# Performance work log

Measured on AMD Instinct MI355X. Metric: run time of the kernel, lower is better.

Reference implementation:

```python
import jax, jax.numpy as jnp
import numpy as np

TAU = 2.0      # LIF membrane time constant
ALPHA = 4.0    # sigmoid surrogate sharpness (spikingjelly default)
EPS = 1e-5     # BatchNorm eps
HEADS = 8


def lif(x, vth):
    """MultiStepLIFNode: scan over leading time dim T. Hard reset to 0, detach_reset.
    Forward spike = heaviside(h - vth); backward uses sigmoid surrogate via straight-through."""
    def step(v, xt):
        h = v + (xt - v) / TAU
        hv = h - vth
        sg = jax.nn.sigmoid(ALPHA * hv)
        hard = (hv >= 0).astype(h.dtype)
        spike = sg + jax.lax.stop_gradient(hard - sg)
        v_new = h * (1.0 - jax.lax.stop_gradient(spike))  # detach_reset=True, v_reset=0
        return v_new, spike
    _, spikes = jax.lax.scan(step, jnp.zeros_like(x[0]), x)
    return spikes


def bn(x, gamma, beta, mean, var):
    # x: (T,B,C,N), params: (C,) ; eval-mode BatchNorm1d over channel axis 2
    inv = (gamma * jax.lax.rsqrt(var + EPS))[None, None, :, None]
    return (x - mean[None, None, :, None]) * inv + beta[None, None, :, None]


def setup_inputs() -> dict:
    key = jax.random.key(0)
    T, B, C, H, W = 4, 16, 384, 32, 32
    ks = jax.random.split(key, 24)
    d = {"x": jax.random.normal(ks[0], (T, B, C, H, W), jnp.float32)}
    i = 1
    wscale = 1.0 / np.sqrt(C)
    for p in ("q", "k", "v", "p"):
        d[p + "_w"] = jax.random.normal(ks[i], (C, C), jnp.float32) * wscale; i += 1
        d[p + "_gamma"] = jax.random.uniform(ks[i], (C,), jnp.float32, 0.5, 1.5); i += 1
        d[p + "_beta"] = jax.random.normal(ks[i], (C,), jnp.float32) * 0.1; i += 1
        d[p + "_mean"] = jax.random.normal(ks[i], (C,), jnp.float32) * 0.1; i += 1
        d[p + "_var"] = jax.random.uniform(ks[i], (C,), jnp.float32, 0.5, 1.5); i += 1
    d["p_bias"] = jax.random.normal(ks[i], (C,), jnp.float32) * 0.1
    return d


def reference(x, q_w, q_gamma, q_beta, q_mean, q_var,
              k_w, k_gamma, k_beta, k_mean, k_var,
              v_w, v_gamma, v_beta, v_mean, v_var,
              p_w, p_bias, p_gamma, p_beta, p_mean, p_var):
    T, B, C, H, W = x.shape
    N = H * W
    Ch = C // HEADS
    # input spiking (named proj_lif in source, applied first)
    xs = lif(x, 1.0).reshape(T, B, C, N)

    def branch(w, g, b, m, v):
        y = jnp.einsum('tbcn,dc->tbdn', xs, w)  # 1x1 Conv1d == channel matmul
        return lif(bn(y, g, b, m, v), 1.0).reshape(T, B, HEADS, Ch, N)

    q = branch(q_w, q_gamma, q_beta, q_mean, q_var)
    k = branch(k_w, k_gamma, k_beta, k_mean, k_var)
    v = branch(v_w, v_gamma, v_beta, v_mean, v_var)

    attn = jnp.sum(k * v, axis=3, keepdims=True)  # (T,B,h,1,N)
    attn = lif(attn, 0.5)
    out = (q * attn).reshape(T, B, C, N)
    out = jnp.einsum('tbcn,dc->tbdn', out, p_w) + p_bias[None, None, :, None]
    out = bn(out, p_gamma, p_beta, p_mean, p_var)
    return out.reshape(T, B, C, H, W)
```

## Files before the change

kernel.cpp:

```cpp
#include <hip/hip_runtime.h>

typedef unsigned short u16;
typedef unsigned char u8;
typedef unsigned int u32;
typedef float f32x4 __attribute__((ext_vector_type(4)));
typedef __bf16 bf16x8 __attribute__((ext_vector_type(8)));

#define SPB 6291456

__device__ __forceinline__ void gll16(const void* g, void* l) {
  __builtin_amdgcn_global_load_lds((const __attribute__((address_space(1))) void*)g,
                                   (__attribute__((address_space(3))) void*)l, 16, 0, 0);
}

__device__ __forceinline__ uint4 expand8f(uint2 v, u32 t) {
  u32 a = (v.x >> t) & 0x01010101u;
  u32 b = (v.y >> t) & 0x01010101u;
  uint4 r;
  r.x = __builtin_amdgcn_perm(0u, a, 0x0C010C00u) * 0x3F80u;
  r.y = __builtin_amdgcn_perm(0u, a, 0x0C030C02u) * 0x3F80u;
  r.z = __builtin_amdgcn_perm(0u, b, 0x0C010C00u) * 0x3F80u;
  r.w = __builtin_amdgcn_perm(0u, b, 0x0C030C02u) * 0x3F80u;
  return r;
}

__global__ __launch_bounds__(256) void k_convert(
    const float* __restrict__ qw, const float* __restrict__ kw,
    const float* __restrict__ vw, const float* __restrict__ pw,
    const float* __restrict__ qg, const float* __restrict__ qbt,
    const float* __restrict__ qm, const float* __restrict__ qv,
    const float* __restrict__ kg, const float* __restrict__ kbt,
    const float* __restrict__ km, const float* __restrict__ kv,
    const float* __restrict__ vg, const float* __restrict__ vbt,
    const float* __restrict__ vm, const float* __restrict__ vv,
    const float* __restrict__ pg, const float* __restrict__ pbt,
    const float* __restrict__ pm, const float* __restrict__ pv,
    const float* __restrict__ pbias,
    u16* __restrict__ Wstk, u16* __restrict__ Pw,
    float4* __restrict__ BNP, float4* __restrict__ PP) {
  int tid = blockIdx.x * 256 + threadIdx.x;
  if (tid < 442368) {
    int r = tid / 384, c = tid - r * 384;
    const float* src = (r < 384) ? qw : (r < 768) ? kw : vw;
    int rr = (r >= 768) ? r - 768 : (r >= 384) ? r - 384 : r;
    unsigned int u = __float_as_uint(src[rr * 384 + c]);
    u = (u + 0x7FFFu + ((u >> 16) & 1u)) >> 16;
    Wstk[tid] = (u16)u;
  } else if (tid < 589824) {
    int i = tid - 442368;
    unsigned int u = __float_as_uint(pw[i]);
    u = (u + 0x7FFFu + ((u >> 16) & 1u)) >> 16;
    Pw[i] = (u16)u;
  } else if (tid < 590976) {
    int r = tid - 589824;
    int br = r / 384, ch = r - br * 384;
    const float* g  = (br == 0) ? qg  : (br == 1) ? kg  : vg;
    const float* bt = (br == 0) ? qbt : (br == 1) ? kbt : vbt;
    const float* m  = (br == 0) ? qm  : (br == 1) ? km  : vm;
    const float* va = (br == 0) ? qv  : (br == 1) ? kv  : vv;
    float inv = g[ch] / sqrtf(va[ch] + 1e-5f);
    BNP[r] = make_float4(inv, m[ch], bt[ch], 0.f);
  } else if (tid < 591360) {
    int ch = tid - 590976;
    float inv = pg[ch] / sqrtf(pv[ch] + 1e-5f);
    PP[ch] = make_float4(inv, pm[ch], pbt[ch], pbias[ch]);
  }
}

__global__ __launch_bounds__(256) void k_lif_in(const float* __restrict__ x, u8* __restrict__ xsb) {
  const int nt = blockIdx.x, ct = blockIdx.y, b = blockIdx.z;
  const int tid = threadIdx.x;
  const int nj = tid & 63, cr = tid >> 6;
  const int c0 = ct * 64, n0 = nt * 64;
  __shared__ u32 nibs[64 * 65];
  float v[16];
  u32 nib[16];
  #pragma unroll
  for (int i = 0; i < 16; ++i) { v[i] = 0.f; nib[i] = 0u; }
  for (int t = 0; t < 4; ++t) {
    const float* xr = x + (((t * 16 + b) * 384 + c0 + cr) * 1024) + n0 + nj;
    #pragma unroll
    for (int it = 0; it < 16; ++it) {
      float xv = xr[it * 4096];
      float vv = v[it];
      float h = __fadd_rn(vv, __fmul_rn(__fsub_rn(xv, vv), 0.5f));
      bool s = h >= 1.f;
      v[it] = s ? 0.f : h;
      nib[it] |= (s ? 1u : 0u) << t;
    }
  }
  #pragma unroll
  for (int it = 0; it < 16; ++it) nibs[nj * 65 + cr + it * 4] = nib[it];
  __syncthreads();
  const int n = tid >> 2, ch = tid & 3;
  u32 w0[4];
  #pragma unroll
  for (int q = 0; q < 4; ++q) {
    u32 acc = 0;
    #pragma unroll
    for (int i = 0; i < 4; ++i)
      acc |= (nibs[n * 65 + ch * 16 + q * 4 + i] & 0xFu) << (8 * i);
    w0[q] = acc;
  }
  *(uint4*)(xsb + ((size_t)(b * 1024 + n0 + n)) * 384 + c0 + ch * 16) =
      make_uint4(w0[0], w0[1], w0[2], w0[3]);
}

#define XLDS_U16 13312
#define WSLOT_U16 4096

#define GISSUE(kt) gll16(Wp + (kt) * 32, &lds[XLDS_U16 + ((kt) % 3) * WSLOT_U16 + wst])

#define MFMA2CI(c0, c1) do { \
    _Pragma("unroll") \
    for (int ci = (c0); ci <= (c1); ++ci) { \
      bf16x8 bw_ = *(const bf16x8*)&wb_[(wcg * 64 + ci * 16 + l15) * 32 + swoff]; \
      _Pragma("unroll") \
      for (int ji = 0; ji < 4; ++ji) \
        acc[ji][ci] = __builtin_amdgcn_mfma_f32_16x16x32_bf16(ax[ji], bw_, acc[ji][ci], 0, 0, 0); \
    } \
  } while (0)

#define GSTEP(t, VN, ISS) do { \
    asm volatile("s_waitcnt vmcnt(" #VN ")" ::: "memory"); \
    __builtin_amdgcn_s_barrier(); \
    asm volatile("" ::: "memory"); \
    ISS; \
    const u8* xb_ = (const u8*)lds; \
    const u16* wb_ = &lds[XLDS_U16 + ((t) % 3) * WSLOT_U16]; \
    bf16x8 ax[4]; \
    _Pragma("unroll") \
    for (int ji = 0; ji < 4; ++ji) { \
      uint2 xr_ = *(const uint2*)(xb_ + (wjg * 16 + ji * 4 + d4) * 416 + (t) * 32 + g8); \
      uint4 e_ = expand8f(xr_, t_lane); \
      ax[ji] = *(bf16x8*)&e_; \
    } \
    __builtin_amdgcn_s_setprio(1); \
    MFMA2CI(0, 1); \
    __builtin_amdgcn_s_setprio(0); \
    __builtin_amdgcn_s_barrier(); \
    asm volatile("" ::: "memory"); \
    __builtin_amdgcn_s_setprio(1); \
    MFMA2CI(2, 3); \
    __builtin_amdgcn_s_setprio(0); \
    __builtin_amdgcn_s_barrier(); \
    asm volatile("" ::: "memory"); \
  } while (0)

#define GEMM_PIPELINE() do { \
    GISSUE(0); GISSUE(1); \
    GSTEP(0, 1, GISSUE(2)); \
    GSTEP(1, 1, GISSUE(3)); \
    GSTEP(2, 1, GISSUE(4)); \
    GSTEP(3, 1, GISSUE(5)); \
    GSTEP(4, 1, GISSUE(6)); \
    GSTEP(5, 1, GISSUE(7)); \
    GSTEP(6, 1, GISSUE(8)); \
    GSTEP(7, 1, GISSUE(9)); \
    GSTEP(8, 1, GISSUE(10)); \
    GSTEP(9, 1, GISSUE(11)); \
    GSTEP(10, 1, ); \
    GSTEP(11, 0, ); \
  } while (0)

#define XSTAGE(XSRC) do { \
    const int xn_ = tid >> 3, xcp_ = tid & 7; \
    const u8* xs_ = (XSRC) + (size_t)(b * 1024 + jt * 64 + xn_) * 384 + xcp_ * 48; \
    u8* xd_ = (u8*)lds + xn_ * 416 + xcp_ * 48; \
    uint4 v0_ = *(const uint4*)(xs_); \
    uint4 v1_ = *(const uint4*)(xs_ + 16); \
    uint4 v2_ = *(const uint4*)(xs_ + 32); \
    *(uint4*)(xd_) = v0_; *(uint4*)(xd_ + 16) = v1_; *(uint4*)(xd_ + 32) = v2_; \
    __syncthreads(); \
  } while (0)

#define GEMM_SETUP() \
  const int tid = threadIdx.x; \
  const int w = tid >> 6, l = tid & 63; \
  const int wjg = w >> 1, wcg = w & 1; \
  const int l15 = tid & 15, g = l >> 4; \
  const int swoff = (g ^ ((l15 >> 1) & 3)) * 8; \
  const int wst = w * 512; \
  const int d4 = l15 >> 2, g8 = g * 8; \
  const u32 t_lane = (u32)(l15 & 3); \
  const int sch = (l & 3) ^ ((l >> 3) & 3); \
  f32x4 acc[4][4]; \
  { const f32x4 zero_ = {0.f, 0.f, 0.f, 0.f}; \
    _Pragma("unroll") \
    for (int ji = 0; ji < 4; ++ji) \
      _Pragma("unroll") \
      for (int ci = 0; ci < 4; ++ci) acc[ji][ci] = zero_; }

__global__ __launch_bounds__(512, 4) void k_qkv(
    const u16* __restrict__ Wstk, const u8* __restrict__ xsb,
    const float4* __restrict__ BNP, u8* __restrict__ sp) {
  const int jt = blockIdx.x, mt = blockIdx.y, b = blockIdx.z;
  __shared__ u16 lds[25600];

  GEMM_SETUP();
  XSTAGE(xsb);

  const int m0 = mt * 128;
  const u16* Wp = Wstk + (size_t)(m0 + w * 16 + (l >> 2)) * 384 + sch * 8;

  GEMM_PIPELINE();

  const int br = mt / 3;
  const int cb = (mt - br * 3) * 128;
  const int n_base = b * 1024 + jt * 64 + wjg * 16 + g;
  u8* spW = sp + (size_t)br * SPB;
  #pragma unroll
  for (int ci = 0; ci < 4; ++ci) {
    const int c_loc = wcg * 64 + ci * 16 + l15;
    float4 pr = BNP[br * 384 + cb + c_loc];
    #pragma unroll
    for (int ji = 0; ji < 4; ++ji) {
      f32x4 a = acc[ji][ci];
      u32 bits = 0;
      float vv = 0.f;
      #pragma unroll
      for (int t = 0; t < 4; ++t) {
        float z = __fadd_rn(__fmul_rn(__fsub_rn(a[t], pr.y), pr.x), pr.z);
        float h = __fadd_rn(vv, __fmul_rn(__fsub_rn(z, vv), 0.5f));
        bool s = h >= 1.f;
        vv = s ? 0.f : h;
        bits |= (s ? 1u : 0u) << t;
      }
      spW[(size_t)(n_base + ji * 4) * 384 + cb + c_loc] = (u8)bits;
    }
  }
}

__global__ __launch_bounds__(256) void k_attn(const u8* __restrict__ sp, u8* __restrict__ xpb) {
  const int gw = blockIdx.x * 4 + (threadIdx.x >> 6);
  const int l = threadIdx.x & 63;
  const int b = gw >> 10, n = gw & 1023;
  const u8* qB = sp;
  const u8* kB = sp + SPB;
  const u8* vB = sp + 2 * SPB;
  const int base = (b * 1024 + n) * 384 + l * 6;
  u16 qu[3], ku[3], vu[3];
  #pragma unroll
  for (int i = 0; i < 3; ++i) {
    qu[i] = *(const u16*)(qB + base + 2 * i);
    ku[i] = *(const u16*)(kB + base + 2 * i);
    vu[i] = *(const u16*)(vB + base + 2 * i);
  }
  u32 s = 0;
  #pragma unroll
  for (int i = 0; i < 3; ++i) {
    u32 a = (u32)(ku[i] & vu[i]);
    #pragma unroll
    for (int t = 0; t < 4; ++t) {
      u32 x = (a >> t) & 0x0101u;
      s += ((x + (x >> 8)) & 3u) << (8 * t);
    }
  }
  s += __shfl_xor(s, 1);
  s += __shfl_xor(s, 2);
  s += __shfl_xor(s, 4);
  float v = 0.f;
  u32 m8 = 0;
  #pragma unroll
  for (int t = 0; t < 4; ++t) {
    float attn = (float)((s >> (8 * t)) & 0xFFu);
    float h = __fadd_rn(v, __fmul_rn(__fsub_rn(attn, v), 0.5f));
    bool sk = h >= 0.5f;
    v = sk ? 0.f : h;
    m8 |= (sk ? 1u : 0u) << t;
  }
  const u16 mm = (u16)(m8 * 0x0101u);
  u16* dst = (u16*)(xpb + base);
  #pragma unroll
  for (int i = 0; i < 3; ++i) dst[i] = qu[i] & mm;
}

__global__ __launch_bounds__(512, 4) void k_proj(
    const u16* __restrict__ Pw, const u8* __restrict__ xpb,
    const float4* __restrict__ PP, float* __restrict__ out) {
  const int jt = blockIdx.x, mt = blockIdx.y, b = blockIdx.z;
  __shared__ u16 lds[25600];

  GEMM_SETUP();
  XSTAGE(xpb);

  const int m0 = mt * 128;
  const u16* Wp = Pw + (size_t)(m0 + w * 16 + (l >> 2)) * 384 + sch * 8;

  GEMM_PIPELINE();

  __syncthreads();
  float* scr = (float*)lds;
  const int n0im = jt * 64;
  float4 prc[4];
  #pragma unroll
  for (int ci = 0; ci < 4; ++ci) prc[ci] = PP[m0 + wcg * 64 + ci * 16 + l15];

  #pragma unroll
  for (int t = 0; t < 4; ++t) {
    #pragma unroll
    for (int ci = 0; ci < 4; ++ci) {
      const int c_loc = wcg * 64 + ci * 16 + l15;
      float4 pr = prc[ci];
      #pragma unroll
      for (int ji = 0; ji < 4; ++ji) {
        const int n_loc = wjg * 16 + ji * 4 + g;
        float zz = __fadd_rn(acc[ji][ci][t], pr.w);
        zz = __fadd_rn(__fmul_rn(__fsub_rn(zz, pr.y), pr.x), pr.z);
        scr[c_loc * 68 + n_loc] = zz;
      }
    }
    __syncthreads();
    #pragma unroll
    for (int it = 0; it < 4; ++it) {
      int slot = tid + it * 512;
      int c = slot >> 4, li = slot & 15;
      float4 val = *(const float4*)&scr[c * 68 + li * 4];
      *(float4*)&out[(((size_t)(t * 16 + b) * 384) + m0 + c) * 1024 + n0im + li * 4] = val;
    }
    __syncthreads();
  }
}

extern "C" void kernel_launch(void* const* d_in, const int* in_sizes, int n_in,
                              void* d_out, int out_size, void* d_ws, size_t ws_size,
                              hipStream_t stream) {
  (void)in_sizes; (void)n_in; (void)out_size; (void)ws_size;
  const float* x   = (const float*)d_in[0];
  const float* qw  = (const float*)d_in[1];
  const float* qg  = (const float*)d_in[2];
  const float* qbt = (const float*)d_in[3];
  const float* qm  = (const float*)d_in[4];
  const float* qv  = (const float*)d_in[5];
  const float* kw  = (const float*)d_in[6];
  const float* kg  = (const float*)d_in[7];
  const float* kbt = (const float*)d_in[8];
  const float* km  = (const float*)d_in[9];
  const float* kv  = (const float*)d_in[10];
  const float* vw  = (const float*)d_in[11];
  const float* vg  = (const float*)d_in[12];
  const float* vbt = (const float*)d_in[13];
  const float* vm  = (const float*)d_in[14];
  const float* vv  = (const float*)d_in[15];
  const float* pw  = (const float*)d_in[16];
  const float* pg  = (const float*)d_in[17];
  const float* pbt = (const float*)d_in[18];
  const float* pm  = (const float*)d_in[19];
  const float* pv  = (const float*)d_in[20];
  const float* pbias = (const float*)d_in[21];

  char* ws = (char*)d_ws;
  u8*  xsb   = (u8*)ws;
  u8*  sp    = (u8*)(ws + 6291456);
  u8*  xpb   = (u8*)(ws + 25165824);
  u16* Wstk  = (u16*)(ws + 31457280);
  u16* Pw    = (u16*)(ws + 32342016);
  float4* BNP = (float4*)(ws + 32636928);
  float4* PP  = (float4*)(ws + 32655360);

  k_convert<<<2310, 256, 0, stream>>>(qw, kw, vw, pw, qg, qbt, qm, qv, kg, kbt, km, kv,
                                      vg, vbt, vm, vv, pg, pbt, pm, pv, pbias,
                                      Wstk, Pw, BNP, PP);
  k_lif_in<<<dim3(16, 6, 16), 256, 0, stream>>>(x, xsb);
  k_qkv<<<dim3(16, 9, 16), 512, 0, stream>>>(Wstk, xsb, BNP, sp);
  k_attn<<<4096, 256, 0, stream>>>(sp, xpb);
  k_proj<<<dim3(16, 3, 16), 512, 0, stream>>>(Pw, xpb, PP, (float*)d_out);
}
```

Measured before the change: 128.9 us.

## Use 256-thread GEMM blocks with each wave covering all 128 output channels

The QKV and projection GEMM kernels move from 512 threads (8 waves split 4x2 over rows and channels) to 256 threads where each of 4 waves computes 16 rows by all 128 channels, doubling accumulators per wave. Each wave now issues two weight loads per k-step and the intra-step mid barriers are removed, so the A fragment is reused across 8 MFMA column tiles instead of 4. This cuts barrier count and redundant X-fragment expansion, at the cost of more registers per thread, lower occupancy and fewer waves to hide latency.

```diff
diff --git a/kernel.cpp b/kernel.cpp
--- a/kernel.cpp
+++ b/kernel.cpp
@@ -109,16 +109,10 @@
 #define XLDS_U16 13312
 #define WSLOT_U16 4096
 
-#define GISSUE(kt) gll16(Wp + (kt) * 32, &lds[XLDS_U16 + ((kt) % 3) * WSLOT_U16 + wst])
-
-#define MFMA2CI(c0, c1) do { \
-    _Pragma("unroll") \
-    for (int ci = (c0); ci <= (c1); ++ci) { \
-      bf16x8 bw_ = *(const bf16x8*)&wb_[(wcg * 64 + ci * 16 + l15) * 32 + swoff]; \
-      _Pragma("unroll") \
-      for (int ji = 0; ji < 4; ++ji) \
-        acc[ji][ci] = __builtin_amdgcn_mfma_f32_16x16x32_bf16(ax[ji], bw_, acc[ji][ci], 0, 0, 0); \
-    } \
+#define GISSUE(kt) do { \
+    u16* wb_ = &lds[XLDS_U16 + ((kt) % 3) * WSLOT_U16 + w * 1024]; \
+    gll16(Wp0 + (kt) * 32, wb_); \
+    gll16(Wp1 + (kt) * 32, wb_ + 512); \
   } while (0)
 
 #define GSTEP(t, VN, ISS) do { \
@@ -131,67 +125,63 @@
     bf16x8 ax[4]; \
     _Pragma("unroll") \
     for (int ji = 0; ji < 4; ++ji) { \
-      uint2 xr_ = *(const uint2*)(xb_ + (wjg * 16 + ji * 4 + d4) * 416 + (t) * 32 + g8); \
+      uint2 xr_ = *(const uint2*)(xb_ + (w * 16 + ji * 4 + d4) * 416 + (t) * 32 + g8); \
       uint4 e_ = expand8f(xr_, t_lane); \
       ax[ji] = *(bf16x8*)&e_; \
     } \
     __builtin_amdgcn_s_setprio(1); \
-    MFMA2CI(0, 1); \
+    _Pragma("unroll") \
+    for (int ci = 0; ci < 8; ++ci) { \
+      bf16x8 bw_ = *(const bf16x8*)&wb_[(ci * 16 + l15) * 32 + swoff]; \
+      _Pragma("unroll") \
+      for (int ji = 0; ji < 4; ++ji) \
+        acc[ji][ci] = __builtin_amdgcn_mfma_f32_16x16x32_bf16(ax[ji], bw_, acc[ji][ci], 0, 0, 0); \
+    } \
     __builtin_amdgcn_s_setprio(0); \
-    __builtin_amdgcn_s_barrier(); \
-    asm volatile("" ::: "memory"); \
-    __builtin_amdgcn_s_setprio(1); \
-    MFMA2CI(2, 3); \
-    __builtin_amdgcn_s_setprio(0); \
-    __builtin_amdgcn_s_barrier(); \
-    asm volatile("" ::: "memory"); \
   } while (0)
 
 #define GEMM_PIPELINE() do { \
     GISSUE(0); GISSUE(1); \
-    GSTEP(0, 1, GISSUE(2)); \
-    GSTEP(1, 1, GISSUE(3)); \
-    GSTEP(2, 1, GISSUE(4)); \
-    GSTEP(3, 1, GISSUE(5)); \
-    GSTEP(4, 1, GISSUE(6)); \
-    GSTEP(5, 1, GISSUE(7)); \
-    GSTEP(6, 1, GISSUE(8)); \
-    GSTEP(7, 1, GISSUE(9)); \
-    GSTEP(8, 1, GISSUE(10)); \
-    GSTEP(9, 1, GISSUE(11)); \
-    GSTEP(10, 1, ); \
+    GSTEP(0, 2, GISSUE(2)); \
+    GSTEP(1, 2, GISSUE(3)); \
+    GSTEP(2, 2, GISSUE(4)); \
+    GSTEP(3, 2, GISSUE(5)); \
+    GSTEP(4, 2, GISSUE(6)); \
+    GSTEP(5, 2, GISSUE(7)); \
+    GSTEP(6, 2, GISSUE(8)); \
+    GSTEP(7, 2, GISSUE(9)); \
+    GSTEP(8, 2, GISSUE(10)); \
+    GSTEP(9, 2, GISSUE(11)); \
+    GSTEP(10, 2, ); \
     GSTEP(11, 0, ); \
   } while (0)
 
 #define XSTAGE(XSRC) do { \
-    const int xn_ = tid >> 3, xcp_ = tid & 7; \
-    const u8* xs_ = (XSRC) + (size_t)(b * 1024 + jt * 64 + xn_) * 384 + xcp_ * 48; \
-    u8* xd_ = (u8*)lds + xn_ * 416 + xcp_ * 48; \
-    uint4 v0_ = *(const uint4*)(xs_); \
-    uint4 v1_ = *(const uint4*)(xs_ + 16); \
-    uint4 v2_ = *(const uint4*)(xs_ + 32); \
-    *(uint4*)(xd_) = v0_; *(uint4*)(xd_ + 16) = v1_; *(uint4*)(xd_ + 32) = v2_; \
+    const int xn_ = tid >> 2, xcp_ = tid & 3; \
+    const u8* xs_ = (XSRC) + (size_t)(b * 1024 + jt * 64 + xn_) * 384 + xcp_ * 96; \
+    u8* xd_ = (u8*)lds + xn_ * 416 + xcp_ * 96; \
+    _Pragma("unroll") \
+    for (int q_ = 0; q_ < 6; ++q_) \
+      *(uint4*)(xd_ + q_ * 16) = *(const uint4*)(xs_ + q_ * 16); \
     __syncthreads(); \
   } while (0)
 
 #define GEMM_SETUP() \
   const int tid = threadIdx.x; \
   const int w = tid >> 6, l = tid & 63; \
-  const int wjg = w >> 1, wcg = w & 1; \
   const int l15 = tid & 15, g = l >> 4; \
   const int swoff = (g ^ ((l15 >> 1) & 3)) * 8; \
-  const int wst = w * 512; \
   const int d4 = l15 >> 2, g8 = g * 8; \
   const u32 t_lane = (u32)(l15 & 3); \
   const int sch = (l & 3) ^ ((l >> 3) & 3); \
-  f32x4 acc[4][4]; \
+  f32x4 acc[4][8]; \
   { const f32x4 zero_ = {0.f, 0.f, 0.f, 0.f}; \
     _Pragma("unroll") \
     for (int ji = 0; ji < 4; ++ji) \
       _Pragma("unroll") \
-      for (int ci = 0; ci < 4; ++ci) acc[ji][ci] = zero_; }
-
-__global__ __launch_bounds__(512, 4) void k_qkv(
+      for (int ci = 0; ci < 8; ++ci) acc[ji][ci] = zero_; }
+
+__global__ __launch_bounds__(256, 2) void k_qkv(
     const u16* __restrict__ Wstk, const u8* __restrict__ xsb,
     const float4* __restrict__ BNP, u8* __restrict__ sp) {
   const int jt = blockIdx.x, mt = blockIdx.y, b = blockIdx.z;
@@ -201,17 +191,18 @@
   XSTAGE(xsb);
 
   const int m0 = mt * 128;
-  const u16* Wp = Wstk + (size_t)(m0 + w * 16 + (l >> 2)) * 384 + sch * 8;
+  const u16* Wp0 = Wstk + (size_t)(m0 + w * 32 + (l >> 2)) * 384 + sch * 8;
+  const u16* Wp1 = Wp0 + 16 * 384;
 
   GEMM_PIPELINE();
 
   const int br = mt / 3;
   const int cb = (mt - br * 3) * 128;
-  const int n_base = b * 1024 + jt * 64 + wjg * 16 + g;
+  const int n_base = b * 1024 + jt * 64 + w * 16 + g;
   u8* spW = sp + (size_t)br * SPB;
   #pragma unroll
-  for (int ci = 0; ci < 4; ++ci) {
-    const int c_loc = wcg * 64 + ci * 16 + l15;
+  for (int ci = 0; ci < 8; ++ci) {
+    const int c_loc = ci * 16 + l15;
     float4 pr = BNP[br * 384 + cb + c_loc];
     #pragma unroll
     for (int ji = 0; ji < 4; ++ji) {
@@ -275,7 +266,7 @@
   for (int i = 0; i < 3; ++i) dst[i] = qu[i] & mm;
 }
 
-__global__ __launch_bounds__(512, 4) void k_proj(
+__global__ __launch_bounds__(256, 2) void k_proj(
     const u16* __restrict__ Pw, const u8* __restrict__ xpb,
     const float4* __restrict__ PP, float* __restrict__ out) {
   const int jt = blockIdx.x, mt = blockIdx.y, b = blockIdx.z;
@@ -285,26 +276,27 @@
   XSTAGE(xpb);
 
   const int m0 = mt * 128;
-  const u16* Wp = Pw + (size_t)(m0 + w * 16 + (l >> 2)) * 384 + sch * 8;
+  const u16* Wp0 = Pw + (size_t)(m0 + w * 32 + (l >> 2)) * 384 + sch * 8;
+  const u16* Wp1 = Wp0 + 16 * 384;
 
   GEMM_PIPELINE();
 
   __syncthreads();
   float* scr = (float*)lds;
   const int n0im = jt * 64;
-  float4 prc[4];
-  #pragma unroll
-  for (int ci = 0; ci < 4; ++ci) prc[ci] = PP[m0 + wcg * 64 + ci * 16 + l15];
+  float4 prc[8];
+  #pragma unroll
+  for (int ci = 0; ci < 8; ++ci) prc[ci] = PP[m0 + ci * 16 + l15];
 
   #pragma unroll
   for (int t = 0; t < 4; ++t) {
     #pragma unroll
-    for (int ci = 0; ci < 4; ++ci) {
-      const int c_loc = wcg * 64 + ci * 16 + l15;
+    for (int ci = 0; ci < 8; ++ci) {
+      const int c_loc = ci * 16 + l15;
       float4 pr = prc[ci];
       #pragma unroll
       for (int ji = 0; ji < 4; ++ji) {
-        const int n_loc = wjg * 16 + ji * 4 + g;
+        const int n_loc = w * 16 + ji * 4 + g;
         float zz = __fadd_rn(acc[ji][ci][t], pr.w);
         zz = __fadd_rn(__fmul_rn(__fsub_rn(zz, pr.y), pr.x), pr.z);
         scr[c_loc * 68 + n_loc] = zz;
@@ -312,8 +304,8 @@
     }
     __syncthreads();
     #pragma unroll
-    for (int it = 0; it < 4; ++it) {
-      int slot = tid + it * 512;
+    for (int it = 0; it < 8; ++it) {
+      int slot = tid + it * 256;
       int c = slot >> 4, li = slot & 15;
       float4 val = *(const float4*)&scr[c * 68 + li * 4];
       *(float4*)&out[(((size_t)(t * 16 + b) * 384) + m0 + c) * 1024 + n0im + li * 4] = val;
@@ -362,7 +354,7 @@
                                       vg, vbt, vm, vv, pg, pbt, pm, pv, pbias,
                                       Wstk, Pw, BNP, PP);
   k_lif_in<<<dim3(16, 6, 16), 256, 0, stream>>>(x, xsb);
-  k_qkv<<<dim3(16, 9, 16), 512, 0, stream>>>(Wstk, xsb, BNP, sp);
+  k_qkv<<<dim3(16, 9, 16), 256, 0, stream>>>(Wstk, xsb, BNP, sp);
   k_attn<<<4096, 256, 0, stream>>>(sp, xpb);
-  k_proj<<<dim3(16, 3, 16), 512, 0, stream>>>(Pw, xpb, PP, (float*)d_out);
-}
+  k_proj<<<dim3(16, 3, 16), 256, 0, stream>>>(Pw, xpb, PP, (float*)d_out);
+}
```

After: 128.7 us. No clear change (-0.2%).
